# Kernel tuning notes

Measured on AMD Instinct MI355X. Metric: run time of the kernel, lower is better.

## Reference

```python
import math
import jax, jax.numpy as jnp
import numpy as np

HEADS = 9
EMBED = 32
TEMPERATURE = 3000.0

def _conv1x1(x, W, b):
    # x: [B,C,H,W], W: [O,C], b: [O]  (1x1 conv == channel matmul)
    return jnp.einsum('bchw,oc->bohw', x, W) + b[None, :, None, None]

def setup_inputs() -> dict:
    key = jax.random.key(0)
    ks = jax.random.split(key, 14)
    B, H, W = 2, 64, 64
    h2, w2 = 32, 32
    hd = HEADS * EMBED  # 288
    s = 0.1
    return {
        'second_frame': jax.random.normal(ks[0], (B, 3, H, W), jnp.float32),
        'first_frame_aligned': jax.random.normal(ks[1], (B, 3, H, W), jnp.float32),
        'second_frame_feat': jax.random.normal(ks[2], (B, 4, h2, w2), jnp.float32),
        'first_frame_feat_aligned': jax.random.normal(ks[3], (B, 4, h2, w2), jnp.float32),
        'Wq': jax.random.normal(ks[4], (hd, 3), jnp.float32) * s,
        'bq': jax.random.normal(ks[5], (hd,), jnp.float32) * s,
        'Wk': jax.random.normal(ks[6], (hd, 3), jnp.float32) * s,
        'bk': jax.random.normal(ks[7], (hd,), jnp.float32) * s,
        'Wv': jax.random.normal(ks[8], (hd, 4), jnp.float32) * s,
        'bv': jax.random.normal(ks[9], (hd,), jnp.float32) * s,
        'Wp': jax.random.normal(ks[10], (4, hd), jnp.float32) * s,
        'bp': jax.random.normal(ks[11], (4,), jnp.float32) * s,
        'Wt': jax.random.normal(ks[12], (1, EMBED), jnp.float32) * s,
        'bt': jax.random.normal(ks[13], (1,), jnp.float32) * s,
    }

def reference(second_frame, first_frame_aligned, second_frame_feat,
              first_frame_feat_aligned, Wq, bq, Wk, bk, Wv, bv, Wp, bp, Wt, bt):
    B, _, H, W = second_frame.shape
    HW = H * W
    # bilinear upsample of aligned features to (H, W); half-pixel centers == align_corners=False
    feat_up = jax.image.resize(first_frame_feat_aligned,
                               (B, first_frame_feat_aligned.shape[1], H, W),
                               method='linear', antialias=False)
    Q = _conv1x1(second_frame, Wq, bq).reshape(B, HEADS, EMBED, HW)
    K = _conv1x1(first_frame_aligned, Wk, bk).reshape(B, HEADS, EMBED, HW)
    V = _conv1x1(feat_up, Wv, bv).reshape(B, HEADS, EMBED, HW)
    Qn = jnp.transpose(Q, (0, 1, 3, 2))                      # [B,h,HW,d]
    sim = jnp.einsum('bhnd,bhdm->bhnm', Qn, K) / math.sqrt(EMBED)  # [B,h,HW,HW]
    # learned per-query threshold from Q
    t = jnp.einsum('bhnd,od->bhno', Qn, Wt) + bt             # [B,h,HW,1]
    attn = jax.nn.relu((sim - t) / TEMPERATURE)              # no row normalization
    out = jnp.einsum('bhnm,bhdm->bhnd', attn, V)             # [B,h,HW,d]
    out = jnp.transpose(out, (0, 1, 3, 2)).reshape(B, HEADS * EMBED, H, W)
    out_feat = _conv1x1(out, Wp, bp)                         # [B,4,H,W]
    h2, w2 = second_frame_feat.shape[-2:]
    out_feat_down = jax.image.resize(out_feat, (B, out_feat.shape[1], h2, w2),
                                     method='linear', antialias=False)
    final_feat = second_frame_feat + out_feat_down
    return final_feat, out_feat_down
```

## Files before the change

kernel.cpp:

```cpp
#include <hip/hip_runtime.h>
#include <hip/hip_bf16.h>
#include <cstddef>

#define NHEADS 9
#define D 32
#define SQ 4096
#define ZSPLIT 8
#define MBLK (SQ / ZSPLIT)
#define CHUNKS (MBLK / 64)
#define KROW 40
#define VROW 72
#define OFCOPY (2 * 4 * SQ)

typedef __attribute__((ext_vector_type(8))) short bf16x8;
typedef __attribute__((ext_vector_type(4))) short bf16x4;
typedef __attribute__((ext_vector_type(4))) float f32x4;

__device__ __forceinline__ unsigned int f2bf(float f) {
    unsigned int u = __float_as_uint(f);
    u += 0x7fffu + ((u >> 16) & 1u);
    return u >> 16;
}

__device__ __forceinline__ void lds_barrier() {
    asm volatile("s_waitcnt lgkmcnt(0)\n\ts_barrier" ::: "memory");
}

__device__ __forceinline__ unsigned int trunc_pk(float lo, float hi) {
    return __builtin_amdgcn_perm(__float_as_uint(hi), __float_as_uint(lo),
                                 0x07060302u);
}

__device__ __forceinline__ bf16x8 relu_pack8(f32x4 s1, f32x4 s2) {
    union { unsigned int u[4]; bf16x8 v; } P;
    P.u[0] = trunc_pk(s1[0], s1[1]);
    P.u[1] = trunc_pk(s1[2], s1[3]);
    P.u[2] = trunc_pk(s2[0], s2[1]);
    P.u[3] = trunc_pk(s2[2], s2[3]);
    const bf16x8 z = {0, 0, 0, 0, 0, 0, 0, 0};
    return __builtin_elementwise_max(P.v, z);
}

__global__ __launch_bounds__(256) void prep_kernel(
    const float* __restrict__ x2, const float* __restrict__ x1,
    const float* __restrict__ feat1,
    const float* __restrict__ Wq, const float* __restrict__ bq,
    const float* __restrict__ Wk, const float* __restrict__ bk,
    const float* __restrict__ Wv, const float* __restrict__ bv,
    const float* __restrict__ Wt, const float* __restrict__ bt,
    unsigned short* __restrict__ Qb, unsigned short* __restrict__ Kb,
    unsigned short* __restrict__ Vt, float* __restrict__ tbuf,
    float* __restrict__ of)
{
    __shared__ unsigned short Vls[32 * 66];

    const int tid = threadIdx.x;
    int idx = blockIdx.x * blockDim.x + tid;
    if (idx < 8 * OFCOPY) of[idx] = 0.0f;
    int g  = idx & 3;
    int nl = tid >> 2;
    int n  = (idx >> 2) & (SQ - 1);
    int bh = idx >> 14;
    int h  = bh % NHEADS;
    int b  = bh / NHEADS;

    float xs0 = x2[((size_t)b * 3 + 0) * SQ + n];
    float xs1 = x2[((size_t)b * 3 + 1) * SQ + n];
    float xs2 = x2[((size_t)b * 3 + 2) * SQ + n];
    float ys0 = x1[((size_t)b * 3 + 0) * SQ + n];
    float ys1 = x1[((size_t)b * 3 + 1) * SQ + n];
    float ys2 = x1[((size_t)b * 3 + 2) * SQ + n];

    int yy = n >> 6, xx = n & 63;
    int jy = yy >> 1, jx = xx >> 1;
    int j0, j1, i0, i1; float wy0, wy1, wx0, wx1;
    if (yy & 1) { j0 = jy; j1 = (jy < 31) ? jy + 1 : 31; wy0 = 0.75f; wy1 = 0.25f; }
    else        { j0 = (jy > 0) ? jy - 1 : 0; j1 = jy;   wy0 = 0.25f; wy1 = 0.75f; }
    if (xx & 1) { i0 = jx; i1 = (jx < 31) ? jx + 1 : 31; wx0 = 0.75f; wx1 = 0.25f; }
    else        { i0 = (jx > 0) ? jx - 1 : 0; i1 = jx;   wx0 = 0.25f; wx1 = 0.75f; }

    float fu[4];
#pragma unroll
    for (int c = 0; c < 4; ++c) {
        const float* f = feat1 + ((size_t)b * 4 + c) * 1024;
        fu[c] = wy0 * (wx0 * f[j0 * 32 + i0] + wx1 * f[j0 * 32 + i1]) +
                wy1 * (wx0 * f[j1 * 32 + i0] + wx1 * f[j1 * 32 + i1]);
    }

    const int d0 = g * 8;
    unsigned int qp[4], kp[4];
    float tpart = 0.0f;
#pragma unroll
    for (int j = 0; j < 8; ++j) {
        int d = d0 + j, hd = h * D + d;
        float q = bq[hd] + Wq[hd * 3] * xs0 + Wq[hd * 3 + 1] * xs1 + Wq[hd * 3 + 2] * xs2;
        float k = bk[hd] + Wk[hd * 3] * ys0 + Wk[hd * 3 + 1] * ys1 + Wk[hd * 3 + 2] * ys2;
        float v = bv[hd] + Wv[hd * 4] * fu[0] + Wv[hd * 4 + 1] * fu[1] +
                  Wv[hd * 4 + 2] * fu[2] + Wv[hd * 4 + 3] * fu[3];
        tpart += q * Wt[d];
        unsigned int qb_ = f2bf(q), kb_ = f2bf(k);
        if (j & 1) { qp[j >> 1] |= qb_ << 16; kp[j >> 1] |= kb_ << 16; }
        else       { qp[j >> 1]  = qb_;       kp[j >> 1]  = kb_; }
        Vls[d * 66 + nl] = (unsigned short)f2bf(v);
    }
    tpart += __shfl_xor(tpart, 1);
    tpart += __shfl_xor(tpart, 2);
    if (g == 0) tbuf[(size_t)bh * SQ + n] = tpart + bt[0];

    size_t base = ((size_t)bh * SQ + n) * D + d0;
    *(uint4*)(Qb + base) = make_uint4(qp[0], qp[1], qp[2], qp[3]);
    *(uint4*)(Kb + base) = make_uint4(kp[0], kp[1], kp[2], kp[3]);

    __syncthreads();
    {
        int r  = tid >> 3;
        int c4 = tid & 7;
        int n0 = (blockIdx.x & 63) * 64;
        unsigned int w0 = *(const unsigned int*)&Vls[r * 66 + c4 * 4];
        unsigned int w1 = *(const unsigned int*)&Vls[r * 66 + c4 * 4 + 2];
        *(uint2*)(Vt + ((size_t)bh * D + r) * SQ + n0 + c4 * 4) = make_uint2(w0, w1);
    }
}

#define COMPUTE(KS, VS)                                                          \
    {                                                                            \
        __builtin_amdgcn_s_setprio(1);                                           \
        _Pragma("unroll")                                                        \
        for (int g32 = 0; g32 < 2; ++g32) {                                      \
            const unsigned short* kbase = KS + g32 * 32 * KROW;                  \
            bf16x8 kf1 = *(const bf16x8*)(kbase + l15 * KROW + quad * 8);        \
            bf16x8 kf2 = *(const bf16x8*)(kbase + (16 + l15) * KROW + quad * 8); \
            bf16x8 vlo = *(const bf16x8*)(VS + l15 * VROW + g32 * 32 + quad * 8);\
            bf16x8 vhi = *(const bf16x8*)(VS + (l15 + 16) * VROW + g32 * 32 + quad * 8);\
            f32x4 sA1 = __builtin_amdgcn_mfma_f32_16x16x32_bf16(kf1, qfA, ciA, 0, 0, 0);\
            f32x4 sA2 = __builtin_amdgcn_mfma_f32_16x16x32_bf16(kf2, qfA, ciA, 0, 0, 0);\
            f32x4 sB1 = __builtin_amdgcn_mfma_f32_16x16x32_bf16(kf1, qfB, ciB, 0, 0, 0);\
            f32x4 sB2 = __builtin_amdgcn_mfma_f32_16x16x32_bf16(kf2, qfB, ciB, 0, 0, 0);\
            f32x4 sC1 = __builtin_amdgcn_mfma_f32_16x16x32_bf16(kf1, qfC, ciC, 0, 0, 0);\
            f32x4 sC2 = __builtin_amdgcn_mfma_f32_16x16x32_bf16(kf2, qfC, ciC, 0, 0, 0);\
            f32x4 sD1 = __builtin_amdgcn_mfma_f32_16x16x32_bf16(kf1, qfD, ciD, 0, 0, 0);\
            f32x4 sD2 = __builtin_amdgcn_mfma_f32_16x16x32_bf16(kf2, qfD, ciD, 0, 0, 0);\
            bf16x8 pA = relu_pack8(sA1, sA2);                                    \
            bf16x8 pB = relu_pack8(sB1, sB2);                                    \
            bf16x8 pC = relu_pack8(sC1, sC2);                                    \
            bf16x8 pD = relu_pack8(sD1, sD2);                                    \
            accAl = __builtin_amdgcn_mfma_f32_16x16x32_bf16(vlo, pA, accAl, 0, 0, 0);\
            accAh = __builtin_amdgcn_mfma_f32_16x16x32_bf16(vhi, pA, accAh, 0, 0, 0);\
            accBl = __builtin_amdgcn_mfma_f32_16x16x32_bf16(vlo, pB, accBl, 0, 0, 0);\
            accBh = __builtin_amdgcn_mfma_f32_16x16x32_bf16(vhi, pB, accBh, 0, 0, 0);\
            accCl = __builtin_amdgcn_mfma_f32_16x16x32_bf16(vlo, pC, accCl, 0, 0, 0);\
            accCh = __builtin_amdgcn_mfma_f32_16x16x32_bf16(vhi, pC, accCh, 0, 0, 0);\
            accDl = __builtin_amdgcn_mfma_f32_16x16x32_bf16(vlo, pD, accDl, 0, 0, 0);\
            accDh = __builtin_amdgcn_mfma_f32_16x16x32_bf16(vhi, pD, accDh, 0, 0, 0);\
        }                                                                        \
        __builtin_amdgcn_s_setprio(0);                                           \
    }

__global__ __launch_bounds__(256, 4) void attn_kernel(
    const unsigned short* __restrict__ Qb,
    const unsigned short* __restrict__ Kb,
    const unsigned short* __restrict__ Vt,
    const float* __restrict__ tbuf,
    const float* __restrict__ Wp,
    float* __restrict__ of)
{
    __shared__ __align__(16) unsigned short Ks0[64 * KROW];
    __shared__ __align__(16) unsigned short Ks1[64 * KROW];
    __shared__ __align__(16) unsigned short Vs0[32 * VROW];
    __shared__ __align__(16) unsigned short Vs1[32 * VROW];

    const int lin  = blockIdx.x;
    const int xcd  = lin & 7;
    const int q8   = lin >> 3;
    const int xblk = q8 & 15;
    const int gl   = q8 >> 4;
    const int grp  = xcd * 18 + gl;
    const int bh   = grp >> 3;
    const int zz   = grp & 7;
    const int h    = bh % NHEADS;
    const int b    = bh / NHEADS;
    const int n0   = xblk * 256;
    const int mc0  = zz * MBLK;
    const int tid  = threadIdx.x;
    const int wave = tid >> 6;
    const int lane = tid & 63;
    const int l15  = lane & 15;
    const int quad = lane >> 4;

    const int nw = n0 + wave * 64;

    const unsigned short* qbase = Qb + ((size_t)bh * SQ + nw + l15) * D + quad * 8;
    bf16x8 qfA = *(const bf16x8*)(qbase);
    bf16x8 qfB = *(const bf16x8*)(qbase + 16 * D);
    bf16x8 qfC = *(const bf16x8*)(qbase + 32 * D);
    bf16x8 qfD = *(const bf16x8*)(qbase + 48 * D);

    const float SQRT32 = 5.656854249492381f;
    const float* tb = tbuf + (size_t)bh * SQ + nw + l15;
    float TA = tb[0]  * SQRT32;
    float TB = tb[16] * SQRT32;
    float TC = tb[32] * SQRT32;
    float TD = tb[48] * SQRT32;
    const f32x4 ciA = {-TA, -TA, -TA, -TA};
    const f32x4 ciB = {-TB, -TB, -TB, -TB};
    const f32x4 ciC = {-TC, -TC, -TC, -TC};
    const f32x4 ciD = {-TD, -TD, -TD, -TD};

    const uint4* Kg4 = (const uint4*)(Kb + (size_t)bh * SQ * D);
    const uint4* Vg4 = (const uint4*)(Vt + (size_t)bh * D * SQ);

    const int krow = tid >> 2;
    const int kcol = (tid & 3) * 8;
    const int kslot = (krow & 32) + 4 * ((krow >> 3) & 3) + (krow & 3) + ((krow & 4) << 2);
    unsigned short* kdst0 = Ks0 + kslot * KROW + kcol;
    unsigned short* kdst1 = Ks1 + kslot * KROW + kcol;
    const int vd = tid >> 3;
    const int vm = (tid & 7) * 8;
    unsigned short* vdst0 = Vs0 + vd * VROW + vm;
    unsigned short* vdst1 = Vs1 + vd * VROW + vm;
    const int vgbase = vd * (SQ / 8) + (mc0 >> 3) + (tid & 7);

    f32x4 accAl = {0.f,0.f,0.f,0.f}, accAh = {0.f,0.f,0.f,0.f};
    f32x4 accBl = {0.f,0.f,0.f,0.f}, accBh = {0.f,0.f,0.f,0.f};
    f32x4 accCl = {0.f,0.f,0.f,0.f}, accCh = {0.f,0.f,0.f,0.f};
    f32x4 accDl = {0.f,0.f,0.f,0.f}, accDh = {0.f,0.f,0.f,0.f};

    uint4 kA = Kg4[(size_t)mc0 * 4 + tid];
    uint4 vA = Vg4[vgbase];
    uint4 kB = Kg4[(size_t)(mc0 + 64) * 4 + tid];
    uint4 vB = Vg4[vgbase + 8];
    *(uint4*)kdst0 = kA;
    *(uint4*)vdst0 = vA;
    kA = Kg4[(size_t)(mc0 + 128) * 4 + tid];
    vA = Vg4[vgbase + 16];
    lds_barrier();

#pragma unroll
    for (int c = 0; c < CHUNKS; c += 2) {
        COMPUTE(Ks0, Vs0);
        *(uint4*)kdst1 = kB;
        *(uint4*)vdst1 = vB;
        {
            const int nc = (c + 3 < CHUNKS) ? c + 3 : CHUNKS - 1;
            kB = Kg4[(size_t)(mc0 + nc * 64) * 4 + tid];
            vB = Vg4[vgbase + nc * 8];
        }
        lds_barrier();

        COMPUTE(Ks1, Vs1);
        if (c + 2 < CHUNKS) {
            *(uint4*)kdst0 = kA;
            *(uint4*)vdst0 = vA;
            const int nc2 = (c + 4 < CHUNKS) ? c + 4 : CHUNKS - 1;
            kA = Kg4[(size_t)(mc0 + nc2 * 64) * 4 + tid];
            vA = Vg4[vgbase + nc2 * 8];
            lds_barrier();
        }
    }

    const float s1 = 5.892556509887896e-05f;
    const float* wph = Wp + h * D + quad * 4;
    float* ofx = of + (size_t)xcd * OFCOPY;
#pragma unroll
    for (int o = 0; o < 4; ++o) {
        float cA = 0.f, cB = 0.f, cC = 0.f, cD = 0.f;
#pragma unroll
        for (int r = 0; r < 4; ++r) {
            float wlo = wph[o * 288 + r], whi = wph[o * 288 + 16 + r];
            cA += accAl[r] * wlo + accAh[r] * whi;
            cB += accBl[r] * wlo + accBh[r] * whi;
            cC += accCl[r] * wlo + accCh[r] * whi;
            cD += accDl[r] * wlo + accDh[r] * whi;
        }
        cA += __shfl_xor(cA, 16); cA += __shfl_xor(cA, 32);
        cB += __shfl_xor(cB, 16); cB += __shfl_xor(cB, 32);
        cC += __shfl_xor(cC, 16); cC += __shfl_xor(cC, 32);
        cD += __shfl_xor(cD, 16); cD += __shfl_xor(cD, 32);
        if (quad == 0) {
            float* ob = &ofx[((size_t)b * 4 + o) * SQ + nw + l15];
            atomicAdd(ob,      cA * s1);
            atomicAdd(ob + 16, cB * s1);
            atomicAdd(ob + 32, cC * s1);
            atomicAdd(ob + 48, cD * s1);
        }
    }
}

__global__ void final_kernel(const float* __restrict__ of,
                             const float* __restrict__ sff,
                             const float* __restrict__ bp,
                             float* __restrict__ dout)
{
    int tid = blockIdx.x * blockDim.x + threadIdx.x;
    if (tid >= 8192) return;
    int i  = tid & 31;
    int jj = (tid >> 5) & 31;
    int bo = tid >> 10;
    int o  = bo & 3;
    int y = jj * 2, x = i * 2;
    float acc = 0.0f;
#pragma unroll
    for (int cp = 0; cp < 8; ++cp) {
        const float* src = of + (size_t)cp * OFCOPY + (size_t)bo * SQ;
        acc += src[y * 64 + x] + src[y * 64 + x + 1] +
               src[(y + 1) * 64 + x] + src[(y + 1) * 64 + x + 1];
    }
    float dval = 0.25f * acc + bp[o];
    dout[tid]        = sff[tid] + dval;
    dout[8192 + tid] = dval;
}

extern "C" void kernel_launch(void* const* d_in, const int* in_sizes, int n_in,
                              void* d_out, int out_size, void* d_ws, size_t ws_size,
                              hipStream_t stream)
{
    const float* second_frame = (const float*)d_in[0];
    const float* first_frame  = (const float*)d_in[1];
    const float* sff          = (const float*)d_in[2];
    const float* ffa          = (const float*)d_in[3];
    const float* Wq = (const float*)d_in[4];
    const float* bq = (const float*)d_in[5];
    const float* Wk = (const float*)d_in[6];
    const float* bk = (const float*)d_in[7];
    const float* Wv = (const float*)d_in[8];
    const float* bv = (const float*)d_in[9];
    const float* Wp = (const float*)d_in[10];
    const float* bp = (const float*)d_in[11];
    const float* Wt = (const float*)d_in[12];
    const float* bt = (const float*)d_in[13];
    float* out = (float*)d_out;

    char* ws = (char*)d_ws;
    const size_t QKV = (size_t)2 * NHEADS * SQ * D * sizeof(unsigned short);
    unsigned short* Qb = (unsigned short*)ws;
    unsigned short* Kb = (unsigned short*)(ws + QKV);
    unsigned short* Vt = (unsigned short*)(ws + 2 * QKV);
    float* tbuf = (float*)(ws + 3 * QKV);
    float* of   = (float*)(ws + 3 * QKV + (size_t)2 * NHEADS * SQ * sizeof(float));

    prep_kernel<<<1152, 256, 0, stream>>>(second_frame, first_frame, ffa,
                                          Wq, bq, Wk, bk, Wv, bv, Wt, bt,
                                          Qb, Kb, Vt, tbuf, of);
    attn_kernel<<<16 * 18 * ZSPLIT, 256, 0, stream>>>(Qb, Kb, Vt, tbuf, Wp, of);
    final_kernel<<<32, 256, 0, stream>>>(of, sff, bp, out);
}
```

Before: 141.5 us.

## Replace atomic partial-sum accumulation with per-split plain stores and parallel reduction

The attention kernel now writes each head/split partial projection to its own slot with plain stores instead of atomicAdd into 8 XCD-replicated buffers. This also drops the zeroing pass from the prep kernel. The final kernel now reduces the 9 heads × 8 splits with 8 threads per output and warp shuffles, across more blocks. The s_setprio hints around the MFMA compute are also removed. The cost is a larger partial buffer (72 slices of 4×4096 floats) that the final kernel must read.

```diff
diff --git a/kernel.cpp b/kernel.cpp
--- a/kernel.cpp
+++ b/kernel.cpp
@@ -10,7 +10,6 @@
 #define CHUNKS (MBLK / 64)
 #define KROW 40
 #define VROW 72
-#define OFCOPY (2 * 4 * SQ)
 
 typedef __attribute__((ext_vector_type(8))) short bf16x8;
 typedef __attribute__((ext_vector_type(4))) short bf16x4;
@@ -49,14 +48,12 @@
     const float* __restrict__ Wv, const float* __restrict__ bv,
     const float* __restrict__ Wt, const float* __restrict__ bt,
     unsigned short* __restrict__ Qb, unsigned short* __restrict__ Kb,
-    unsigned short* __restrict__ Vt, float* __restrict__ tbuf,
-    float* __restrict__ of)
+    unsigned short* __restrict__ Vt, float* __restrict__ tbuf)
 {
     __shared__ unsigned short Vls[32 * 66];
 
     const int tid = threadIdx.x;
     int idx = blockIdx.x * blockDim.x + tid;
-    if (idx < 8 * OFCOPY) of[idx] = 0.0f;
     int g  = idx & 3;
     int nl = tid >> 2;
     int n  = (idx >> 2) & (SQ - 1);
@@ -124,7 +121,6 @@
 
 #define COMPUTE(KS, VS)                                                          \
     {                                                                            \
-        __builtin_amdgcn_s_setprio(1);                                           \
         _Pragma("unroll")                                                        \
         for (int g32 = 0; g32 < 2; ++g32) {                                      \
             const unsigned short* kbase = KS + g32 * 32 * KROW;                  \
@@ -153,7 +149,6 @@
             accDl = __builtin_amdgcn_mfma_f32_16x16x32_bf16(vlo, pD, accDl, 0, 0, 0);\
             accDh = __builtin_amdgcn_mfma_f32_16x16x32_bf16(vhi, pD, accDh, 0, 0, 0);\
         }                                                                        \
-        __builtin_amdgcn_s_setprio(0);                                           \
     }
 
 __global__ __launch_bounds__(256, 4) void attn_kernel(
@@ -162,7 +157,7 @@
     const unsigned short* __restrict__ Vt,
     const float* __restrict__ tbuf,
     const float* __restrict__ Wp,
-    float* __restrict__ of)
+    float* __restrict__ ofp)
 {
     __shared__ __align__(16) unsigned short Ks0[64 * KROW];
     __shared__ __align__(16) unsigned short Ks1[64 * KROW];
@@ -178,7 +173,6 @@
     const int bh   = grp >> 3;
     const int zz   = grp & 7;
     const int h    = bh % NHEADS;
-    const int b    = bh / NHEADS;
     const int n0   = xblk * 256;
     const int mc0  = zz * MBLK;
     const int tid  = threadIdx.x;
@@ -260,7 +254,7 @@
 
     const float s1 = 5.892556509887896e-05f;
     const float* wph = Wp + h * D + quad * 4;
-    float* ofx = of + (size_t)xcd * OFCOPY;
+    float* obase = ofp + ((size_t)(bh * 8 + zz) * 4) * SQ + nw + l15;
 #pragma unroll
     for (int o = 0; o < 4; ++o) {
         float cA = 0.f, cB = 0.f, cC = 0.f, cD = 0.f;
@@ -277,37 +271,46 @@
         cC += __shfl_xor(cC, 16); cC += __shfl_xor(cC, 32);
         cD += __shfl_xor(cD, 16); cD += __shfl_xor(cD, 32);
         if (quad == 0) {
-            float* ob = &ofx[((size_t)b * 4 + o) * SQ + nw + l15];
-            atomicAdd(ob,      cA * s1);
-            atomicAdd(ob + 16, cB * s1);
-            atomicAdd(ob + 32, cC * s1);
-            atomicAdd(ob + 48, cD * s1);
+            float* ob = obase + (size_t)o * SQ;
+            ob[0]  = cA * s1;
+            ob[16] = cB * s1;
+            ob[32] = cC * s1;
+            ob[48] = cD * s1;
         }
     }
 }
 
-__global__ void final_kernel(const float* __restrict__ of,
-                             const float* __restrict__ sff,
-                             const float* __restrict__ bp,
-                             float* __restrict__ dout)
+__global__ __launch_bounds__(256) void final_kernel(
+    const float* __restrict__ ofp,
+    const float* __restrict__ sff,
+    const float* __restrict__ bp,
+    float* __restrict__ dout)
 {
-    int tid = blockIdx.x * blockDim.x + threadIdx.x;
-    if (tid >= 8192) return;
-    int i  = tid & 31;
-    int jj = (tid >> 5) & 31;
-    int bo = tid >> 10;
+    int t = blockIdx.x * 256 + threadIdx.x;
+    int out = t >> 3;
+    int s   = t & 7;
+    int i  = out & 31;
+    int jj = (out >> 5) & 31;
+    int bo = out >> 10;
     int o  = bo & 3;
-    int y = jj * 2, x = i * 2;
+    int b  = bo >> 2;
+    int nbase = (jj * 2) * 64 + i * 2;
+
     float acc = 0.0f;
 #pragma unroll
-    for (int cp = 0; cp < 8; ++cp) {
-        const float* src = of + (size_t)cp * OFCOPY + (size_t)bo * SQ;
-        acc += src[y * 64 + x] + src[y * 64 + x + 1] +
-               src[(y + 1) * 64 + x] + src[(y + 1) * 64 + x + 1];
-    }
-    float dval = 0.25f * acc + bp[o];
-    dout[tid]        = sff[tid] + dval;
-    dout[8192 + tid] = dval;
+    for (int h = 0; h < NHEADS; ++h) {
+        const float* src = ofp +
+            ((size_t)(((b * NHEADS + h) * 8 + s) * 4 + o)) * SQ + nbase;
+        acc += src[0] + src[1] + src[64] + src[65];
+    }
+    acc += __shfl_xor(acc, 1);
+    acc += __shfl_xor(acc, 2);
+    acc += __shfl_xor(acc, 4);
+    if (s == 0) {
+        float dval = 0.25f * acc + bp[o];
+        dout[out]        = sff[out] + dval;
+        dout[8192 + out] = dval;
+    }
 }
 
 extern "C" void kernel_launch(void* const* d_in, const int* in_sizes, int n_in,
@@ -336,11 +339,11 @@
     unsigned short* Kb = (unsigned short*)(ws + QKV);
     unsigned short* Vt = (unsigned short*)(ws + 2 * QKV);
     float* tbuf = (float*)(ws + 3 * QKV);
-    float* of   = (float*)(ws + 3 * QKV + (size_t)2 * NHEADS * SQ * sizeof(float));
+    float* ofp  = (float*)(ws + 3 * QKV + (size_t)2 * NHEADS * SQ * sizeof(float));
 
     prep_kernel<<<1152, 256, 0, stream>>>(second_frame, first_frame, ffa,
                                           Wq, bq, Wk, bk, Wv, bv, Wt, bt,
-                                          Qb, Kb, Vt, tbuf, of);
-    attn_kernel<<<16 * 18 * ZSPLIT, 256, 0, stream>>>(Qb, Kb, Vt, tbuf, Wp, of);
-    final_kernel<<<32, 256, 0, stream>>>(of, sff, bp, out);
-}
+                                          Qb, Kb, Vt, tbuf);
+    attn_kernel<<<16 * 18 * ZSPLIT, 256, 0, stream>>>(Qb, Kb, Vt, tbuf, Wp, ofp);
+    final_kernel<<<256, 256, 0, stream>>>(ofp, sff, bp, out);
+}
```

Result: faster. 135.2 us (-4.4%).
